# Kernel optimization log

Hardware: AMD Instinct MI355X
Metric: run time of the kernel (lower is better)

The kernel has to match this reference:

```python
import jax, jax.numpy as jnp
import numpy as np

VOCAB, EMB, HID = 32000, 1024, 1024
SEQ, BATCH = 512, 64


def setup_inputs() -> dict:
    key = jax.random.key(0)
    ks = jax.random.split(key, 8)
    inp = {
        "input": jax.random.randint(ks[0], (SEQ, BATCH), 0, VOCAB, dtype=jnp.int64)
        if jax.config.jax_enable_x64 else jax.random.randint(ks[0], (SEQ, BATCH), 0, VOCAB, dtype=jnp.int32),
        "input_lengths": jax.random.randint(ks[1], (BATCH,), 1, SEQ, dtype=jnp.int32),
        "hidden": jnp.zeros((1, BATCH, HID), dtype=jnp.float32),
        # parameters (xavier-ish scaled normals)
        "emb": jax.random.normal(ks[2], (VOCAB, EMB), dtype=jnp.float32) * (2.0 / (VOCAB + EMB)) ** 0.5,
        "W_ih": jax.random.normal(ks[3], (3 * HID, EMB), dtype=jnp.float32) * (1.0 / HID) ** 0.5,
        "W_hh": jax.random.normal(ks[4], (3 * HID, HID), dtype=jnp.float32) * (1.0 / HID) ** 0.5,
        "b_ih": jax.random.normal(ks[5], (3 * HID,), dtype=jnp.float32) * (1.0 / HID) ** 0.5,
        "b_hh": jax.random.normal(ks[6], (3 * HID,), dtype=jnp.float32) * (1.0 / HID) ** 0.5,
    }
    return inp


def _gru_scan(x, h0, W_ih, W_hh, b_ih, b_hh):
    # x: (T, B, D); h0: (B, H). PyTorch GRU gate math, gates ordered r, z, n.
    H = h0.shape[-1]

    def step(h, x_t):
        gi = x_t @ W_ih.T + b_ih          # (B, 3H)
        gh = h @ W_hh.T + b_hh            # (B, 3H)
        i_r, i_z, i_n = gi[:, :H], gi[:, H:2 * H], gi[:, 2 * H:]
        h_r, h_z, h_n = gh[:, :H], gh[:, H:2 * H], gh[:, 2 * H:]
        r = jax.nn.sigmoid(i_r + h_r)
        z = jax.nn.sigmoid(i_z + h_z)
        n = jnp.tanh(i_n + r * h_n)
        h_new = (1.0 - z) * n + z * h
        return h_new, h_new

    _, hs = jax.lax.scan(step, h0, x)
    return hs  # (T, B, H)


def reference(input, input_lengths, hidden, emb, W_ih, W_hh, b_ih, b_hh):
    # embedded: (T, B, D); input_lengths is unused by the original forward.
    embedded = emb[input]
    h0 = hidden[0]  # num_layers == 1
    hiddens = _gru_scan(embedded, h0, W_ih, W_hh, b_ih, b_hh)
    # torch.stack(hidden_list, 0).squeeze(1) with num_layers=1 -> (T, B, H)
    return hiddens
```

## Files before the change

### kernel.cpp

```cpp
#include <hip/hip_runtime.h>

typedef short bhalf8 __attribute__((ext_vector_type(8)));
typedef float f32x4  __attribute__((ext_vector_type(4)));

__device__ __forceinline__ unsigned short f2bf(float f) {
    unsigned int u = __builtin_bit_cast(unsigned int, f);
    u = (u + 0x7fffu + ((u >> 16) & 1u)) >> 16;
    return (unsigned short)u;
}
__device__ __forceinline__ float bf2f(unsigned short h) {
    unsigned int u = ((unsigned int)h) << 16;
    return __builtin_bit_cast(float, u);
}

__device__ __forceinline__ bhalf8 ldg16_bypass(const unsigned short* p) {
    bhalf8 r;
    asm volatile("global_load_dwordx4 %0, %1, off sc0 sc1"
                 : "=v"(r) : "v"(p));
    return r;
}

#define VWAIT(N)                                                     \
    do {                                                             \
        asm volatile("s_waitcnt vmcnt(" #N ")" ::: "memory");        \
        __builtin_amdgcn_sched_barrier(0);                           \
    } while (0)

#define SEQ   512
#define BATCH 64
#define HID   1024
#define EMBD  1024
#define VOCAB 32000
#define N3H   3072
#define NBLK  64
#define FLAGSTRIDE 32

__global__ void k_cvt4(const float4* __restrict__ in, ushort4* __restrict__ out, int n4) {
    int i = blockIdx.x * blockDim.x + threadIdx.x;
    if (i < n4) {
        float4 v = in[i];
        ushort4 o;
        o.x = f2bf(v.x); o.y = f2bf(v.y); o.z = f2bf(v.z); o.w = f2bf(v.w);
        out[i] = o;
    }
}

__global__ __launch_bounds__(256)
void k_gi(const int* __restrict__ tok, const unsigned short* __restrict__ embb,
          const unsigned short* __restrict__ wih, unsigned short* __restrict__ gi) {
    int nb = blockIdx.x;
    int mb = blockIdx.y;
    int w    = threadIdx.x >> 6;
    int lane = threadIdx.x & 63;
    int q = lane >> 4, l = lane & 15;
    int m0 = mb * 256 + w * 16;
    int n0 = nb * 64;

    const unsigned short* ap[4];
#pragma unroll
    for (int i = 0; i < 4; ++i)
        ap[i] = embb + (size_t)tok[m0 + 64 * i + l] * EMBD + q * 8;

    const unsigned short* bp[4];
#pragma unroll
    for (int j = 0; j < 4; ++j)
        bp[j] = wih + (size_t)(n0 + 16 * j + l) * EMBD + q * 8;

    f32x4 acc[4][4];
#pragma unroll
    for (int i = 0; i < 4; ++i)
#pragma unroll
        for (int j = 0; j < 4; ++j)
            acc[i][j] = (f32x4){0.f, 0.f, 0.f, 0.f};

#pragma unroll 2
    for (int kk = 0; kk < 32; ++kk) {
        int ko = kk * 32;
        bhalf8 bv[4], av[4];
#pragma unroll
        for (int j = 0; j < 4; ++j) bv[j] = *(const bhalf8*)(bp[j] + ko);
#pragma unroll
        for (int i = 0; i < 4; ++i) av[i] = *(const bhalf8*)(ap[i] + ko);
#pragma unroll
        for (int i = 0; i < 4; ++i)
#pragma unroll
            for (int j = 0; j < 4; ++j)
                acc[i][j] = __builtin_amdgcn_mfma_f32_16x16x32_bf16(av[i], bv[j], acc[i][j], 0, 0, 0);
    }
#pragma unroll
    for (int i = 0; i < 4; ++i)
#pragma unroll
        for (int r = 0; r < 4; ++r) {
            size_t mrow = (size_t)(m0 + 64 * i + q * 4 + r) * N3H + n0;
            gi[mrow +  0 + l] = f2bf(acc[i][0][r]);
            gi[mrow + 16 + l] = f2bf(acc[i][1][r]);
            gi[mrow + 32 + l] = f2bf(acc[i][2][r]);
            gi[mrow + 48 + l] = f2bf(acc[i][3][r]);
        }
}

__device__ __forceinline__ void gbar(int* flags, int e) {
    __syncthreads();
    if (threadIdx.x == 0)
        __hip_atomic_store(flags + (size_t)blockIdx.x * FLAGSTRIDE, e,
                           __ATOMIC_RELAXED, __HIP_MEMORY_SCOPE_AGENT);
    if (threadIdx.x < 64) {
        for (;;) {
            int v = __hip_atomic_load(flags + (size_t)threadIdx.x * FLAGSTRIDE,
                                      __ATOMIC_RELAXED, __HIP_MEMORY_SCOPE_AGENT);
            if (__all(v >= e)) break;
            __builtin_amdgcn_s_sleep(1);
        }
    }
    __syncthreads();
}

__global__ __launch_bounds__(256, 1)
void k_rec(const float* __restrict__ W_hh,
           const unsigned short* __restrict__ gib,
           const float* __restrict__ bih, const float* __restrict__ bhh,
           const float* __restrict__ hidden,
           float* __restrict__ out,
           unsigned short* hbuf,
           int* flags) {
    __shared__ unsigned short sh[32768];

    const int tid  = threadIdx.x;
    const int w    = tid >> 6;
    const int lane = tid & 63;
    const int q = lane >> 4, l = lane & 15;
    const int G  = blockIdx.x;
    const int m0 = w * 16;
    const int u0 = G * 16 + l;

    for (int i = 0; i < 16; ++i) {
        int c  = i * 256 + tid;
        int g  = c >> 11;
        int kk = (c >> 6) & 31;
        int ln = c & 63;
        int uu = ln & 15, qq = ln >> 4;
        const float* src = W_hh + (size_t)(g * 1024 + G * 16 + uu) * 1024 + kk * 32 + qq * 8;
        float4 f0 = *(const float4*)src;
        float4 f1 = *(const float4*)(src + 4);
        ushort4 o0, o1;
        o0.x = f2bf(f0.x); o0.y = f2bf(f0.y); o0.z = f2bf(f0.z); o0.w = f2bf(f0.w);
        o1.x = f2bf(f1.x); o1.y = f2bf(f1.y); o1.z = f2bf(f1.z); o1.w = f2bf(f1.w);
        *(ushort4*)&sh[c * 8]     = o0;
        *(ushort4*)&sh[c * 8 + 4] = o1;
    }

    bhalf8 bn[32];
#pragma unroll
    for (int kk = 0; kk < 32; ++kk) {
        const float* src = W_hh + (size_t)(2048 + u0) * 1024 + kk * 32 + q * 8;
        float4 f0 = *(const float4*)src;
        float4 f1 = *(const float4*)(src + 4);
        bhalf8 v;
        v[0] = (short)f2bf(f0.x); v[1] = (short)f2bf(f0.y);
        v[2] = (short)f2bf(f0.z); v[3] = (short)f2bf(f0.w);
        v[4] = (short)f2bf(f1.x); v[5] = (short)f2bf(f1.y);
        v[6] = (short)f2bf(f1.z); v[7] = (short)f2bf(f1.w);
        bn[kk] = v;
    }

    float hp[4];
#pragma unroll
    for (int r = 0; r < 4; ++r) {
        int b = m0 + q * 4 + r;
        float hv = hidden[(size_t)b * HID + u0];
        hp[r] = hv;
        __hip_atomic_store(hbuf + (size_t)b * HID + u0, f2bf(hv),
                           __ATOMIC_RELAXED, __HIP_MEMORY_SCOPE_AGENT);
    }
    float bir = bih[u0], biz = bih[HID + u0], bin = bih[2 * HID + u0];
    float bhr = bhh[u0], bhz = bhh[HID + u0], bhn = bhh[2 * HID + u0];

    float i_r[4], i_z[4], i_n[4];
#pragma unroll
    for (int r = 0; r < 4; ++r) {
        const unsigned short* gp = gib + (size_t)(m0 + q * 4 + r) * N3H + u0;
        i_r[r] = bf2f(gp[0])       + bir;
        i_z[r] = bf2f(gp[HID])     + biz;
        i_n[r] = bf2f(gp[2 * HID]) + bin;
    }

    gbar(flags, 1);

#define ISSUE8(AV, KB)                                                   \
    _Pragma("unroll")                                                    \
    for (int j = 0; j < 8; ++j) AV[j] = ldg16_bypass(hA + ((KB) + j) * 32);

#define COMPUTE8(AV, KB)                                                 \
    _Pragma("unroll")                                                    \
    for (int j = 0; j < 8; ++j) {                                        \
        int kk = (KB) + j;                                               \
        bhalf8 brf = *(const bhalf8*)&sh[kk * 512 + lane * 8];           \
        bhalf8 bzf = *(const bhalf8*)&sh[16384 + kk * 512 + lane * 8];   \
        ar = __builtin_amdgcn_mfma_f32_16x16x32_bf16(AV[j], brf, ar, 0, 0, 0); \
        az = __builtin_amdgcn_mfma_f32_16x16x32_bf16(AV[j], bzf, az, 0, 0, 0); \
        an = __builtin_amdgcn_mfma_f32_16x16x32_bf16(AV[j], bn[kk], an, 0, 0, 0); \
    }

    for (int t = 0; t < SEQ; ++t) {
        const unsigned short* hc = hbuf + (size_t)(t & 1) * (BATCH * HID);
        unsigned short*       hn = hbuf + (size_t)((t + 1) & 1) * (BATCH * HID);

        unsigned short pr[4], pz[4], pn[4];
        if (t + 1 < SEQ) {
            const unsigned short* gt = gib + (size_t)(t + 1) * (BATCH * N3H);
#pragma unroll
            for (int r = 0; r < 4; ++r) {
                const unsigned short* gp = gt + (size_t)(m0 + q * 4 + r) * N3H + u0;
                pr[r] = gp[0]; pz[r] = gp[HID]; pn[r] = gp[2 * HID];
            }
        }

        const unsigned short* hA = hc + (size_t)(m0 + l) * HID + q * 8;
        f32x4 ar = {0.f, 0.f, 0.f, 0.f}, az = ar, an = ar;

        {
            bhalf8 ha[8], hb[8];
            ISSUE8(ha, 0)
            ISSUE8(hb, 8)
            VWAIT(8);
            COMPUTE8(ha, 0)
            ISSUE8(ha, 16)
            VWAIT(8);
            COMPUTE8(hb, 8)
            ISSUE8(hb, 24)
            VWAIT(8);
            COMPUTE8(ha, 16)
            VWAIT(0);
            COMPUTE8(hb, 24)
        }

        float osv[4];
#pragma unroll
        for (int r = 0; r < 4; ++r) {
            int b = m0 + q * 4 + r;
            float rr = 1.f / (1.f + __expf(-(i_r[r] + ar[r] + bhr)));
            float zz = 1.f / (1.f + __expf(-(i_z[r] + az[r] + bhz)));
            float nn = tanhf(i_n[r] + rr * (an[r] + bhn));
            float hv = (1.f - zz) * nn + zz * hp[r];
            hp[r] = hv;
            osv[r] = hv;
            if (t + 1 < SEQ)
                __hip_atomic_store(hn + (size_t)b * HID + u0, f2bf(hv),
                                   __ATOMIC_RELAXED, __HIP_MEMORY_SCOPE_AGENT);
        }

        if (t + 1 < SEQ) {
#pragma unroll
            for (int r = 0; r < 4; ++r) {
                i_r[r] = bf2f(pr[r]) + bir;
                i_z[r] = bf2f(pz[r]) + biz;
                i_n[r] = bf2f(pn[r]) + bin;
            }
            gbar(flags, t + 2);
        }

        float* ot = out + (size_t)t * (BATCH * HID);
#pragma unroll
        for (int r = 0; r < 4; ++r)
            __builtin_nontemporal_store(osv[r], &ot[(size_t)(m0 + q * 4 + r) * HID + u0]);
    }
#undef ISSUE8
#undef COMPUTE8
}

extern "C" void kernel_launch(void* const* d_in, const int* in_sizes, int n_in,
                              void* d_out, int out_size, void* d_ws, size_t ws_size,
                              hipStream_t stream) {
    (void)in_sizes; (void)n_in; (void)out_size;
    const int*   input  = (const int*)  d_in[0];
    const float* hidden = (const float*)d_in[2];
    const float* emb    = (const float*)d_in[3];
    const float* W_ih   = (const float*)d_in[4];
    const float* W_hh   = (const float*)d_in[5];
    const float* b_ih   = (const float*)d_in[6];
    const float* b_hh   = (const float*)d_in[7];
    float* out = (float*)d_out;

    const size_t EMB_BF  = 0;
    const size_t WIH_BF  = EMB_BF + (size_t)VOCAB * EMBD * 2;
    const size_t GI_OFF  = WIH_BF + (size_t)N3H * EMBD * 2;
    const size_t H_OFF   = GI_OFF + (size_t)SEQ * BATCH * N3H * 2;
    const size_t FLG_OFF = H_OFF + (size_t)2 * BATCH * HID * 2;
    const size_t NEED    = FLG_OFF + (size_t)NBLK * FLAGSTRIDE * 4;
    if (ws_size < NEED) return;

    char* ws = (char*)d_ws;
    unsigned short* embb = (unsigned short*)(ws + EMB_BF);
    unsigned short* wihb = (unsigned short*)(ws + WIH_BF);
    unsigned short* gib  = (unsigned short*)(ws + GI_OFF);
    unsigned short* hbuf = (unsigned short*)(ws + H_OFF);
    int*            flags = (int*)(ws + FLG_OFF);

    hipMemsetAsync(flags, 0, (size_t)NBLK * FLAGSTRIDE * 4, stream);

    {
        int n4 = VOCAB * EMBD / 4;
        k_cvt4<<<(n4 + 255) / 256, 256, 0, stream>>>((const float4*)emb, (ushort4*)embb, n4);
    }
    {
        int n4 = N3H * EMBD / 4;
        k_cvt4<<<(n4 + 255) / 256, 256, 0, stream>>>((const float4*)W_ih, (ushort4*)wihb, n4);
    }

    k_gi<<<dim3(48, 128), 256, 0, stream>>>(input, embb, wihb, gib);

    k_rec<<<NBLK, 256, 0, stream>>>(W_hh, gib, b_ih, b_hh, hidden, out, hbuf, flags);
}
```

Baseline: 4.279 ms.

## Issue all hidden-state loads upfront and defer output stores past the barrier

Each timestep now issues all 32 hidden-state vector loads at once, followed by the next step's gate-input loads as inline asm, and waits on vmcnt in stages instead of using a two-buffer ping-pong. The output for step t-1 is stored at the start of step t, with the final step written after the loop. This takes the global stores off the critical path before the grid barrier and overlaps load latency with compute. It raises register pressure (four 8-vector buffers) and depends on hand-counted vmcnt values that must match the issue order exactly.

```diff
diff --git a/kernel.cpp b/kernel.cpp
--- a/kernel.cpp
+++ b/kernel.cpp
@@ -201,40 +201,50 @@
         an = __builtin_amdgcn_mfma_f32_16x16x32_bf16(AV[j], bn[kk], an, 0, 0, 0); \
     }
 
+    float osv[4] = {0.f, 0.f, 0.f, 0.f};
+
     for (int t = 0; t < SEQ; ++t) {
         const unsigned short* hc = hbuf + (size_t)(t & 1) * (BATCH * HID);
         unsigned short*       hn = hbuf + (size_t)((t + 1) & 1) * (BATCH * HID);
-
-        unsigned short pr[4], pz[4], pn[4];
-        if (t + 1 < SEQ) {
-            const unsigned short* gt = gib + (size_t)(t + 1) * (BATCH * N3H);
+        const unsigned short* hA = hc + (size_t)(m0 + l) * HID + q * 8;
+
+        f32x4 ar = {0.f, 0.f, 0.f, 0.f}, az = ar, an = ar;
+
+        bhalf8 ha[8], hb[8], hcv[8], hd[8];
+        ISSUE8(ha,  0)
+        ISSUE8(hb,  8)
+        ISSUE8(hcv, 16)
+        ISSUE8(hd,  24)
+
+        unsigned int pr[4], pz[4], pn[4];
+        {
+            const unsigned short* gt = gib +
+                (size_t)((t + 1 < SEQ) ? (t + 1) : t) * (BATCH * N3H);
 #pragma unroll
             for (int r = 0; r < 4; ++r) {
                 const unsigned short* gp = gt + (size_t)(m0 + q * 4 + r) * N3H + u0;
-                pr[r] = gp[0]; pz[r] = gp[HID]; pn[r] = gp[2 * HID];
+                asm volatile("global_load_ushort %0, %1, off" : "=v"(pr[r]) : "v"(gp));
+                asm volatile("global_load_ushort %0, %1, off" : "=v"(pz[r]) : "v"(gp + HID));
+                asm volatile("global_load_ushort %0, %1, off" : "=v"(pn[r]) : "v"(gp + 2 * HID));
             }
         }
 
-        const unsigned short* hA = hc + (size_t)(m0 + l) * HID + q * 8;
-        f32x4 ar = {0.f, 0.f, 0.f, 0.f}, az = ar, an = ar;
-
         {
-            bhalf8 ha[8], hb[8];
-            ISSUE8(ha, 0)
-            ISSUE8(hb, 8)
-            VWAIT(8);
-            COMPUTE8(ha, 0)
-            ISSUE8(ha, 16)
-            VWAIT(8);
-            COMPUTE8(hb, 8)
-            ISSUE8(hb, 24)
-            VWAIT(8);
-            COMPUTE8(ha, 16)
-            VWAIT(0);
-            COMPUTE8(hb, 24)
-        }
-
-        float osv[4];
+            float* ot = out + (size_t)(t ? t - 1 : 0) * (BATCH * HID);
+#pragma unroll
+            for (int r = 0; r < 4; ++r) {
+                float* op = &ot[(size_t)(m0 + q * 4 + r) * HID + u0];
+                asm volatile("global_store_dword %0, %1, off"
+                             :: "v"(op), "v"(osv[r]) : "memory");
+            }
+        }
+
+        VWAIT(40);  COMPUTE8(ha,  0)
+        VWAIT(32);  COMPUTE8(hb,  8)
+        VWAIT(24);  COMPUTE8(hcv, 16)
+        VWAIT(16);  COMPUTE8(hd,  24)
+        VWAIT(4);
+
 #pragma unroll
         for (int r = 0; r < 4; ++r) {
             int b = m0 + q * 4 + r;
@@ -249,20 +259,21 @@
                                    __ATOMIC_RELAXED, __HIP_MEMORY_SCOPE_AGENT);
         }
 
-        if (t + 1 < SEQ) {
-#pragma unroll
-            for (int r = 0; r < 4; ++r) {
-                i_r[r] = bf2f(pr[r]) + bir;
-                i_z[r] = bf2f(pz[r]) + biz;
-                i_n[r] = bf2f(pn[r]) + bin;
-            }
-            gbar(flags, t + 2);
-        }
-
-        float* ot = out + (size_t)t * (BATCH * HID);
+#pragma unroll
+        for (int r = 0; r < 4; ++r) {
+            i_r[r] = bf2f((unsigned short)pr[r]) + bir;
+            i_z[r] = bf2f((unsigned short)pz[r]) + biz;
+            i_n[r] = bf2f((unsigned short)pn[r]) + bin;
+        }
+
+        if (t + 1 < SEQ) gbar(flags, t + 2);
+    }
+
+    {
+        float* ot = out + (size_t)(SEQ - 1) * (BATCH * HID);
 #pragma unroll
         for (int r = 0; r < 4; ++r)
-            __builtin_nontemporal_store(osv[r], &ot[(size_t)(m0 + q * 4 + r) * HID + u0]);
+            ot[(size_t)(m0 + q * 4 + r) * HID + u0] = osv[r];
     }
 #undef ISSUE8
 #undef COMPUTE8
```

Result: slower. 4.598 ms (+7.5%).
